# Kernel optimization log

Measured on AMD Instinct MI355X. Metric: run time of the kernel, lower is better.

The kernel has to match this reference:

```python
import jax, jax.numpy as jnp
import numpy as np

K = 6            # kmer length
NF = 8192        # n_filters (> 4**K so kmer_params has shape (NF, 4, K))
M = 4 ** K       # 4096 kmers
B = 1024         # batch


def setup_inputs() -> dict:
    key = jax.random.key(0)
    k1, k2 = jax.random.split(key)
    freq = jax.random.uniform(k1, (B, M), dtype=jnp.float32)          # kmer frequencies (B, 4^k)
    kmer_params = jax.random.normal(k2, (NF, 4, K), dtype=jnp.float32)
    temperature = jnp.ones((1,), dtype=jnp.float32)
    # base-4 digits of arange(4^k), most-significant first == itertools.product order
    pos = 4 ** jnp.arange(K - 1, -1, -1)
    kmer_idcs = ((jnp.arange(M)[:, None] // pos[None, :]) % 4).astype(jnp.int32)  # (M, K)
    return {"freq": freq, "kmer_params": kmer_params,
            "temperature": temperature, "kmer_idcs": kmer_idcs}


def reference(freq, kmer_params, temperature, kmer_idcs):
    k = kmer_params.shape[-1]
    # matches[f, i] = sum_j kmer_params[f, kmer_idcs[i, j], j]
    # Advanced indexing broadcasts (M, k) indices against arange(k): result (F, M, k).
    # This replaces torch's expand-to-(F, M, 1, k) + gather + squeeze + sum(-1).
    matches = kmer_params[:, kmer_idcs, jnp.arange(k)].sum(axis=-1)   # (F, M)
    probs = jax.nn.softmax(matches / temperature, axis=1)             # softmax over kmers
    pooled = freq @ probs.T                                           # (B, F)
    profile = pooled / pooled.sum(axis=1, keepdims=True)
    return profile
```

## Files before the change

### kernel.cpp

```cpp
#include <hip/hip_runtime.h>


typedef __bf16  bf16x8 __attribute__((ext_vector_type(8)));
typedef float   f32x4  __attribute__((ext_vector_type(4)));

#define GLD16(gp, lp)                                                          \
  __builtin_amdgcn_global_load_lds(                                            \
      (const __attribute__((address_space(1))) void*)(gp),                     \
      (__attribute__((address_space(3))) void*)(lp), 16, 0, 0)

__device__ __forceinline__ short f2bf(float x) {
  unsigned u = __float_as_uint(x);
  unsigned r = (u + 0x7fffu + ((u >> 16) & 1u)) >> 16;
  return (short)r;
}

__device__ __forceinline__ float wave_max(float v) {
  #pragma unroll
  for (int off = 32; off; off >>= 1) v = fmaxf(v, __shfl_xor(v, off, 64));
  return v;
}
__device__ __forceinline__ float wave_sum(float v) {
  #pragma unroll
  for (int off = 32; off; off >>= 1) v += __shfl_xor(v, off, 64);
  return v;
}

__global__ __launch_bounds__(256) void cast_kernel(const float* __restrict__ in,
                                                   short* __restrict__ out) {
  int idx = blockIdx.x * 256 + threadIdx.x;
  float4 v = ((const float4*)in)[idx];
  short4 o;
  o.x = f2bf(v.x); o.y = f2bf(v.y); o.z = f2bf(v.z); o.w = f2bf(v.w);
  ((short4*)out)[idx] = o;
}

__global__ __launch_bounds__(256) void tables_kernel(const float* __restrict__ kp,
                                                     const float* __restrict__ temp,
                                                     float* __restrict__ E1t,
                                                     float* __restrict__ E2) {
  const int t = threadIdx.x;
  const int lane = t & 63, wave = t >> 6;
  const int f = blockIdx.x * 4 + wave;
  const float* P = kp + f * 24;
  const int d0 = (lane >> 4) & 3, d1 = (lane >> 2) & 3, d2 = lane & 3;
  const float thi = P[d0 * 6 + 0] + P[d1 * 6 + 1] + P[d2 * 6 + 2];
  const float tlo = P[d0 * 6 + 3] + P[d1 * 6 + 4] + P[d2 * 6 + 5];
  const float mxhi = wave_max(thi), mxlo = wave_max(tlo);
  const float invT = 1.0f / temp[0];
  const float e1 = __expf((thi - mxhi) * invT);
  const float e2 = __expf((tlo - mxlo) * invT);
  const float s1 = wave_sum(e1), s2 = wave_sum(e2);
  const float invZ = 1.0f / (s1 * s2);
  E1t[lane * 8192 + f] = e1 * invZ;
  E2[(size_t)f * 64 + lane] = e2;
}

__global__ __launch_bounds__(256, 4) void gemm_kernel(const short* __restrict__ A,
                                                      const float* __restrict__ E1t,
                                                      const float* __restrict__ E2,
                                                      float* __restrict__ C) {
  __shared__ short As[64 * 64];

  const int t = threadIdx.x;
  const int lane = t & 63, wave = t >> 6;
  const int quad = lane >> 4, l16 = lane & 15;
  const int m0 = blockIdx.y * 64;
  const int n0 = blockIdx.x * 128;
  const int wn = wave * 32;

  f32x4 acc[4][2];
  #pragma unroll
  for (int i = 0; i < 4; i++)
    #pragma unroll
    for (int j = 0; j < 2; j++) acc[i][j] = (f32x4){0.f, 0.f, 0.f, 0.f};

  int nrow[2];
  #pragma unroll
  for (int j = 0; j < 2; j++) nrow[j] = n0 + wn + j * 16 + l16;
  float4 e2a[2][2], e2b[2][2];
  #pragma unroll
  for (int j = 0; j < 2; j++)
    #pragma unroll
    for (int ks = 0; ks < 2; ks++) {
      const float* p = E2 + (size_t)nrow[j] * 64 + (ks * 4 + quad) * 8;
      e2a[j][ks] = *(const float4*)p;
      e2b[j][ks] = *(const float4*)(p + 4);
    }

  const int lane_row = lane >> 3;
  const int src_col = ((lane & 7) ^ lane_row) * 8;
  const int sw = l16 & 7;

  for (int kt = 0; kt < 64; kt++) {
    const int kofs = kt * 64;
    float e1v[2];
    #pragma unroll
    for (int j = 0; j < 2; j++) e1v[j] = E1t[kt * 8192 + nrow[j]];

    __syncthreads();
    #pragma unroll
    for (int c = 0; c < 2; c++) {
      const int chunk = wave * 2 + c;
      const int row = chunk * 8 + lane_row;
      GLD16(A + (m0 + row) * 4096 + kofs + src_col, &As[chunk * 512 + lane * 8]);
    }
    __syncthreads();

    bf16x8 b[2][2];
    #pragma unroll
    for (int j = 0; j < 2; j++)
      #pragma unroll
      for (int ks = 0; ks < 2; ks++) {
        const float s = e1v[j];
        bf16x8 bb;
        bb[0] = (__bf16)(s * e2a[j][ks].x);
        bb[1] = (__bf16)(s * e2a[j][ks].y);
        bb[2] = (__bf16)(s * e2a[j][ks].z);
        bb[3] = (__bf16)(s * e2a[j][ks].w);
        bb[4] = (__bf16)(s * e2b[j][ks].x);
        bb[5] = (__bf16)(s * e2b[j][ks].y);
        bb[6] = (__bf16)(s * e2b[j][ks].z);
        bb[7] = (__bf16)(s * e2b[j][ks].w);
        b[ks][j] = bb;
      }

    #pragma unroll
    for (int ks = 0; ks < 2; ks++) {
      const int pcol = ((ks * 4 + quad) ^ sw) * 8;
      bf16x8 a[4];
      #pragma unroll
      for (int i = 0; i < 4; i++)
        a[i] = *(const bf16x8*)&As[(i * 16 + l16) * 64 + pcol];
      #pragma unroll
      for (int i = 0; i < 4; i++)
        #pragma unroll
        for (int j = 0; j < 2; j++)
          acc[i][j] = __builtin_amdgcn_mfma_f32_16x16x32_bf16(a[i], b[ks][j], acc[i][j], 0, 0, 0);
    }
  }

  #pragma unroll
  for (int i = 0; i < 4; i++) {
    #pragma unroll
    for (int r = 0; r < 4; r++) {
      const int brow = m0 + i * 16 + quad * 4 + r;
      float* crow = C + (size_t)brow * 8192 + n0 + wn + l16;
      #pragma unroll
      for (int j = 0; j < 2; j++) crow[j * 16] = acc[i][j][r];
    }
  }
}

__global__ __launch_bounds__(256) void norm_kernel(float* __restrict__ out) {
  const int b = blockIdx.x;
  const int t = threadIdx.x;
  const int lane = t & 63, wave = t >> 6;
  __shared__ float red[4];

  float4* row = (float4*)(out + (size_t)b * 8192);
  float4 v[8];
  float s = 0.0f;
  #pragma unroll
  for (int q = 0; q < 8; q++) {
    v[q] = row[q * 256 + t];
    s += (v[q].x + v[q].y) + (v[q].z + v[q].w);
  }
  float ws = wave_sum(s);
  if (lane == 0) red[wave] = ws;
  __syncthreads();
  float tot = (red[0] + red[1]) + (red[2] + red[3]);
  float inv = 1.0f / tot;
  #pragma unroll
  for (int q = 0; q < 8; q++) {
    v[q].x *= inv; v[q].y *= inv; v[q].z *= inv; v[q].w *= inv;
    row[q * 256 + t] = v[q];
  }
}

extern "C" void kernel_launch(void* const* d_in, const int* in_sizes, int n_in,
                              void* d_out, int out_size, void* d_ws, size_t ws_size,
                              hipStream_t stream) {
  const float* freq    = (const float*)d_in[0];
  const float* kparams = (const float*)d_in[1];
  const float* temp    = (const float*)d_in[2];

  float* out = (float*)d_out;

  short* freqb = (short*)d_ws;
  float* E1t   = (float*)(freqb + (size_t)1024 * 4096);
  float* E2    = E1t + (size_t)64 * 8192;

  cast_kernel  <<<4096, 256, 0, stream>>>(freq, freqb);
  tables_kernel<<<2048, 256, 0, stream>>>(kparams, temp, E1t, E2);
  gemm_kernel  <<<dim3(64, 16), 256, 0, stream>>>(freqb, E1t, E2, out);
  norm_kernel  <<<1024, 256, 0, stream>>>(out);
}
```

Baseline: 162.1 us.

## Precompute row denominators algebraically and fuse normalization into GEMM epilogue

Merges the cast and table kernels into one prep kernel that also computes per-block partial column sums of the bf16-rounded probability matrix. A new denom kernel reduces these sums and dots them with each freq row to get the row normalizer ahead of time. The GEMM then scales its output directly, so the separate norm pass that re-read and rewrote the 32MB output disappears. The cost is an extra small kernel with only 64 blocks and an extra reduction inside prep. The normalizer is now computed from rounded values rather than from the GEMM output, so it may differ slightly from the actual row sums.

```diff
diff --git a/kernel.cpp b/kernel.cpp
--- a/kernel.cpp
+++ b/kernel.cpp
@@ -14,6 +14,14 @@
   unsigned r = (u + 0x7fffu + ((u >> 16) & 1u)) >> 16;
   return (short)r;
 }
+__device__ __forceinline__ float bf_round(float x) {
+  unsigned u = __float_as_uint(x);
+  unsigned r = (u + 0x7fffu + ((u >> 16) & 1u)) & 0xffff0000u;
+  return __uint_as_float(r);
+}
+__device__ __forceinline__ float bf2f(unsigned short u) {
+  return __uint_as_float(((unsigned)u) << 16);
+}
 
 __device__ __forceinline__ float wave_max(float v) {
   #pragma unroll
@@ -26,39 +34,134 @@
   return v;
 }
 
-__global__ __launch_bounds__(256) void cast_kernel(const float* __restrict__ in,
-                                                   short* __restrict__ out) {
-  int idx = blockIdx.x * 256 + threadIdx.x;
-  float4 v = ((const float4*)in)[idx];
-  short4 o;
-  o.x = f2bf(v.x); o.y = f2bf(v.y); o.z = f2bf(v.z); o.w = f2bf(v.w);
-  ((short4*)out)[idx] = o;
-}
-
-__global__ __launch_bounds__(256) void tables_kernel(const float* __restrict__ kp,
-                                                     const float* __restrict__ temp,
-                                                     float* __restrict__ E1t,
-                                                     float* __restrict__ E2) {
+__global__ __launch_bounds__(256) void prep_kernel(const float* __restrict__ freq,
+                                                   const float* __restrict__ kp,
+                                                   const float* __restrict__ temp,
+                                                   short* __restrict__ freqb,
+                                                   float* __restrict__ E1t,
+                                                   float* __restrict__ E2,
+                                                   float* __restrict__ S_part) {
+  __shared__ float E1loc[64][64];
+  __shared__ float E2loc[64][64];
+  const int blk = blockIdx.x;
   const int t = threadIdx.x;
+
+  if (blk < 4096) {
+    int idx = blk * 256 + t;
+    float4 v = ((const float4*)freq)[idx];
+    short4 o;
+    o.x = f2bf(v.x); o.y = f2bf(v.y); o.z = f2bf(v.z); o.w = f2bf(v.w);
+    ((short4*)freqb)[idx] = o;
+    return;
+  }
+
+  const int bb = blk - 4096;
+  const int f0 = bb * 64;
   const int lane = t & 63, wave = t >> 6;
-  const int f = blockIdx.x * 4 + wave;
-  const float* P = kp + f * 24;
+  const float invT = 1.0f / temp[0];
   const int d0 = (lane >> 4) & 3, d1 = (lane >> 2) & 3, d2 = lane & 3;
-  const float thi = P[d0 * 6 + 0] + P[d1 * 6 + 1] + P[d2 * 6 + 2];
-  const float tlo = P[d0 * 6 + 3] + P[d1 * 6 + 4] + P[d2 * 6 + 5];
-  const float mxhi = wave_max(thi), mxlo = wave_max(tlo);
-  const float invT = 1.0f / temp[0];
-  const float e1 = __expf((thi - mxhi) * invT);
-  const float e2 = __expf((tlo - mxlo) * invT);
-  const float s1 = wave_sum(e1), s2 = wave_sum(e2);
-  const float invZ = 1.0f / (s1 * s2);
-  E1t[lane * 8192 + f] = e1 * invZ;
-  E2[(size_t)f * 64 + lane] = e2;
+
+  #pragma unroll
+  for (int ffi = 0; ffi < 16; ffi++) {
+    const int floc = wave * 16 + ffi;
+    const float* P = kp + (size_t)(f0 + floc) * 24;
+    const float thi = P[d0 * 6 + 0] + P[d1 * 6 + 1] + P[d2 * 6 + 2];
+    const float tlo = P[d0 * 6 + 3] + P[d1 * 6 + 4] + P[d2 * 6 + 5];
+    const float mxhi = wave_max(thi), mxlo = wave_max(tlo);
+    const float e1 = __expf((thi - mxhi) * invT);
+    const float e2 = __expf((tlo - mxlo) * invT);
+    const float s1 = wave_sum(e1), s2 = wave_sum(e2);
+    const float invZ = 1.0f / (s1 * s2);
+    E1loc[floc][lane] = e1 * invZ;
+    E2loc[floc][lane] = e2;
+  }
+  __syncthreads();
+
+  {
+    const int h = t >> 2, lb = (t & 3) * 16;
+    float acc[16];
+    #pragma unroll
+    for (int ll = 0; ll < 16; ll++) acc[ll] = 0.0f;
+    for (int ff = 0; ff < 64; ff++) {
+      const float a = E1loc[ff][h];
+      #pragma unroll
+      for (int ll = 0; ll < 16; ll++)
+        acc[ll] += bf_round(a * E2loc[ff][lb + ll]);
+    }
+    float* dst = S_part + (size_t)bb * 4096 + h * 64 + lb;
+    #pragma unroll
+    for (int q = 0; q < 4; q++)
+      ((f32x4*)dst)[q] = (f32x4){acc[q*4], acc[q*4+1], acc[q*4+2], acc[q*4+3]};
+  }
+
+  {
+    const int h = t >> 2, c0 = (t & 3) * 16;
+    float tmp[16];
+    #pragma unroll
+    for (int cc = 0; cc < 16; cc++) tmp[cc] = E1loc[c0 + cc][h];
+    float* dst = E1t + (size_t)h * 8192 + f0 + c0;
+    #pragma unroll
+    for (int q = 0; q < 4; q++)
+      ((f32x4*)dst)[q] = (f32x4){tmp[q*4], tmp[q*4+1], tmp[q*4+2], tmp[q*4+3]};
+  }
+
+  {
+    const int fl = t >> 2, l0 = (t & 3) * 16;
+    float* dst = E2 + (size_t)(f0 + fl) * 64 + l0;
+    #pragma unroll
+    for (int q = 0; q < 4; q++)
+      ((f32x4*)dst)[q] = *(const f32x4*)&E2loc[fl][l0 + q * 4];
+  }
+}
+
+__global__ __launch_bounds__(256) void denom_kernel(const short* __restrict__ freqb,
+                                                    const float* __restrict__ S_part,
+                                                    float* __restrict__ invDenom) {
+  __shared__ float Svec[4096];
+  const int t = threadIdx.x;
+  const int b0 = blockIdx.x * 16;
+
+  {
+    const int i0 = t * 16;
+    float acc[16];
+    #pragma unroll
+    for (int q = 0; q < 16; q++) acc[q] = 0.0f;
+    for (int p = 0; p < 128; p++) {
+      const f32x4* src = (const f32x4*)(S_part + (size_t)p * 4096 + i0);
+      #pragma unroll
+      for (int q = 0; q < 4; q++) {
+        f32x4 v = src[q];
+        acc[q*4+0] += v.x; acc[q*4+1] += v.y; acc[q*4+2] += v.z; acc[q*4+3] += v.w;
+      }
+    }
+    #pragma unroll
+    for (int q = 0; q < 4; q++)
+      ((f32x4*)(Svec + i0))[q] = (f32x4){acc[q*4], acc[q*4+1], acc[q*4+2], acc[q*4+3]};
+  }
+  __syncthreads();
+
+  const int lane = t & 63, wave = t >> 6;
+  #pragma unroll
+  for (int rr = 0; rr < 4; rr++) {
+    const int row = b0 + wave * 4 + rr;
+    const unsigned short* fr = (const unsigned short*)(freqb + (size_t)row * 4096);
+    float s = 0.0f;
+    #pragma unroll
+    for (int ch = 0; ch < 16; ch++) {
+      const int i = ch * 256 + lane * 4;
+      ushort4 u = *(const ushort4*)(fr + i);
+      f32x4 sv = *(const f32x4*)(Svec + i);
+      s += bf2f(u.x) * sv.x + bf2f(u.y) * sv.y + bf2f(u.z) * sv.z + bf2f(u.w) * sv.w;
+    }
+    const float tot = wave_sum(s);
+    if (lane == 0) invDenom[row] = 1.0f / tot;
+  }
 }
 
 __global__ __launch_bounds__(256, 4) void gemm_kernel(const short* __restrict__ A,
                                                       const float* __restrict__ E1t,
                                                       const float* __restrict__ E2,
+                                                      const float* __restrict__ invDenom,
                                                       float* __restrict__ C) {
   __shared__ short As[64 * 64];
 
@@ -140,6 +243,13 @@
     }
   }
 
+  float invd[4][4];
+  #pragma unroll
+  for (int i = 0; i < 4; i++)
+    #pragma unroll
+    for (int r = 0; r < 4; r++)
+      invd[i][r] = invDenom[m0 + i * 16 + quad * 4 + r];
+
   #pragma unroll
   for (int i = 0; i < 4; i++) {
     #pragma unroll
@@ -147,34 +257,8 @@
       const int brow = m0 + i * 16 + quad * 4 + r;
       float* crow = C + (size_t)brow * 8192 + n0 + wn + l16;
       #pragma unroll
-      for (int j = 0; j < 2; j++) crow[j * 16] = acc[i][j][r];
-    }
-  }
-}
-
-__global__ __launch_bounds__(256) void norm_kernel(float* __restrict__ out) {
-  const int b = blockIdx.x;
-  const int t = threadIdx.x;
-  const int lane = t & 63, wave = t >> 6;
-  __shared__ float red[4];
-
-  float4* row = (float4*)(out + (size_t)b * 8192);
-  float4 v[8];
-  float s = 0.0f;
-  #pragma unroll
-  for (int q = 0; q < 8; q++) {
-    v[q] = row[q * 256 + t];
-    s += (v[q].x + v[q].y) + (v[q].z + v[q].w);
-  }
-  float ws = wave_sum(s);
-  if (lane == 0) red[wave] = ws;
-  __syncthreads();
-  float tot = (red[0] + red[1]) + (red[2] + red[3]);
-  float inv = 1.0f / tot;
-  #pragma unroll
-  for (int q = 0; q < 8; q++) {
-    v[q].x *= inv; v[q].y *= inv; v[q].z *= inv; v[q].w *= inv;
-    row[q * 256 + t] = v[q];
+      for (int j = 0; j < 2; j++) crow[j * 16] = acc[i][j][r] * invd[i][r];
+    }
   }
 }
 
@@ -190,9 +274,10 @@
   short* freqb = (short*)d_ws;
   float* E1t   = (float*)(freqb + (size_t)1024 * 4096);
   float* E2    = E1t + (size_t)64 * 8192;
-
-  cast_kernel  <<<4096, 256, 0, stream>>>(freq, freqb);
-  tables_kernel<<<2048, 256, 0, stream>>>(kparams, temp, E1t, E2);
-  gemm_kernel  <<<dim3(64, 16), 256, 0, stream>>>(freqb, E1t, E2, out);
-  norm_kernel  <<<1024, 256, 0, stream>>>(out);
-}
+  float* S_part = E2 + (size_t)8192 * 64;
+  float* invDenom = S_part + (size_t)128 * 4096;
+
+  prep_kernel <<<4224, 256, 0, stream>>>(freq, kparams, temp, freqb, E1t, E2, S_part);
+  denom_kernel<<<64, 256, 0, stream>>>(freqb, S_part, invDenom);
+  gemm_kernel <<<dim3(64, 16), 256, 0, stream>>>(freqb, E1t, E2, invDenom, out);
+}
```

New measurement: 228.7 us. 41.1% more time.

## Fuse cast and table kernels, coalesce E1t writes, deepen GEMM K-tile

Applied to the files above, without the earlier changes.

Merges the bf16 cast and the softmax-table kernels into one launch. Table blocks now handle 64 filters each and stage the results in shared memory so the transposed E1t writes go out as coalesced vector stores. The GEMM K-tile grows from 64 to 256, which cuts the number of barrier pairs and per-iteration global loads by four. In exchange it uses four times the LDS (32KB) and lowers the launch-bounds occupancy hint to 3.

```diff
diff --git a/kernel.cpp b/kernel.cpp
--- a/kernel.cpp
+++ b/kernel.cpp
@@ -26,41 +26,73 @@
   return v;
 }
 
-__global__ __launch_bounds__(256) void cast_kernel(const float* __restrict__ in,
-                                                   short* __restrict__ out) {
-  int idx = blockIdx.x * 256 + threadIdx.x;
-  float4 v = ((const float4*)in)[idx];
-  short4 o;
-  o.x = f2bf(v.x); o.y = f2bf(v.y); o.z = f2bf(v.z); o.w = f2bf(v.w);
-  ((short4*)out)[idx] = o;
-}
-
-__global__ __launch_bounds__(256) void tables_kernel(const float* __restrict__ kp,
-                                                     const float* __restrict__ temp,
-                                                     float* __restrict__ E1t,
-                                                     float* __restrict__ E2) {
+__global__ __launch_bounds__(256) void prep_kernel(const float* __restrict__ freq,
+                                                   const float* __restrict__ kp,
+                                                   const float* __restrict__ temp,
+                                                   short* __restrict__ freqb,
+                                                   float* __restrict__ E1t,
+                                                   float* __restrict__ E2) {
+  __shared__ float E1loc[64][64];
+  __shared__ float E2loc[64][64];
+  const int blk = blockIdx.x;
   const int t = threadIdx.x;
+
+  if (blk < 4096) {
+    int idx = blk * 256 + t;
+    float4 v = ((const float4*)freq)[idx];
+    short4 o;
+    o.x = f2bf(v.x); o.y = f2bf(v.y); o.z = f2bf(v.z); o.w = f2bf(v.w);
+    ((short4*)freqb)[idx] = o;
+    return;
+  }
+
+  const int bb = blk - 4096;
+  const int f0 = bb * 64;
   const int lane = t & 63, wave = t >> 6;
-  const int f = blockIdx.x * 4 + wave;
-  const float* P = kp + f * 24;
+  const float invT = 1.0f / temp[0];
   const int d0 = (lane >> 4) & 3, d1 = (lane >> 2) & 3, d2 = lane & 3;
-  const float thi = P[d0 * 6 + 0] + P[d1 * 6 + 1] + P[d2 * 6 + 2];
-  const float tlo = P[d0 * 6 + 3] + P[d1 * 6 + 4] + P[d2 * 6 + 5];
-  const float mxhi = wave_max(thi), mxlo = wave_max(tlo);
-  const float invT = 1.0f / temp[0];
-  const float e1 = __expf((thi - mxhi) * invT);
-  const float e2 = __expf((tlo - mxlo) * invT);
-  const float s1 = wave_sum(e1), s2 = wave_sum(e2);
-  const float invZ = 1.0f / (s1 * s2);
-  E1t[lane * 8192 + f] = e1 * invZ;
-  E2[(size_t)f * 64 + lane] = e2;
-}
-
-__global__ __launch_bounds__(256, 4) void gemm_kernel(const short* __restrict__ A,
+
+  #pragma unroll
+  for (int ffi = 0; ffi < 16; ffi++) {
+    const int floc = wave * 16 + ffi;
+    const float* P = kp + (size_t)(f0 + floc) * 24;
+    const float thi = P[d0 * 6 + 0] + P[d1 * 6 + 1] + P[d2 * 6 + 2];
+    const float tlo = P[d0 * 6 + 3] + P[d1 * 6 + 4] + P[d2 * 6 + 5];
+    const float mxhi = wave_max(thi), mxlo = wave_max(tlo);
+    const float e1 = __expf((thi - mxhi) * invT);
+    const float e2 = __expf((tlo - mxlo) * invT);
+    const float s1 = wave_sum(e1), s2 = wave_sum(e2);
+    const float invZ = 1.0f / (s1 * s2);
+    E1loc[floc][lane] = e1 * invZ;
+    E2loc[floc][lane] = e2;
+  }
+  __syncthreads();
+
+  {
+    const int h = t >> 2, c0 = (t & 3) * 16;
+    float tmp[16];
+    #pragma unroll
+    for (int cc = 0; cc < 16; cc++) tmp[cc] = E1loc[c0 + cc][h];
+    float* dst = E1t + (size_t)h * 8192 + f0 + c0;
+    #pragma unroll
+    for (int q = 0; q < 4; q++)
+      ((f32x4*)dst)[q] = (f32x4){tmp[q*4], tmp[q*4+1], tmp[q*4+2], tmp[q*4+3]};
+  }
+
+  {
+    const int fl = t >> 2, l0 = (t & 3) * 16;
+    float* dst = E2 + (size_t)(f0 + fl) * 64 + l0;
+    #pragma unroll
+    for (int q = 0; q < 4; q++)
+      ((f32x4*)dst)[q] = *(const f32x4*)&E2loc[fl][l0 + q * 4];
+  }
+}
+
+__global__ __launch_bounds__(256, 3) void gemm_kernel(const short* __restrict__ A,
                                                       const float* __restrict__ E1t,
                                                       const float* __restrict__ E2,
                                                       float* __restrict__ C) {
-  __shared__ short As[64 * 64];
+  __shared__ short As[64 * 256];
 
   const int t = threadIdx.x;
   const int lane = t & 63, wave = t >> 6;
@@ -78,65 +110,72 @@
   int nrow[2];
   #pragma unroll
   for (int j = 0; j < 2; j++) nrow[j] = n0 + wn + j * 16 + l16;
+
   float4 e2a[2][2], e2b[2][2];
   #pragma unroll
   for (int j = 0; j < 2; j++)
     #pragma unroll
-    for (int ks = 0; ks < 2; ks++) {
-      const float* p = E2 + (size_t)nrow[j] * 64 + (ks * 4 + quad) * 8;
-      e2a[j][ks] = *(const float4*)p;
-      e2b[j][ks] = *(const float4*)(p + 4);
-    }
-
-  const int lane_row = lane >> 3;
-  const int src_col = ((lane & 7) ^ lane_row) * 8;
+    for (int par = 0; par < 2; par++) {
+      const float* p = E2 + (size_t)nrow[j] * 64 + par * 32 + quad * 8;
+      e2a[j][par] = *(const float4*)p;
+      e2b[j][par] = *(const float4*)(p + 4);
+    }
+
+  const int lrow_half = lane >> 5;
+  const int pblk = lane & 31;
   const int sw = l16 & 7;
 
-  for (int kt = 0; kt < 64; kt++) {
-    const int kofs = kt * 64;
-    float e1v[2];
-    #pragma unroll
-    for (int j = 0; j < 2; j++) e1v[j] = E1t[kt * 8192 + nrow[j]];
+  for (int kt = 0; kt < 16; kt++) {
+    const int kofs = kt * 256;
+
+    float e1v[2][4];
+    #pragma unroll
+    for (int hh = 0; hh < 4; hh++)
+      #pragma unroll
+      for (int j = 0; j < 2; j++)
+        e1v[j][hh] = E1t[(kt * 4 + hh) * 8192 + nrow[j]];
 
     __syncthreads();
     #pragma unroll
-    for (int c = 0; c < 2; c++) {
-      const int chunk = wave * 2 + c;
-      const int row = chunk * 8 + lane_row;
+    for (int c = 0; c < 8; c++) {
+      const int chunk = wave * 8 + c;
+      const int row = chunk * 2 + lrow_half;
+      const int src_col = (pblk ^ (row & 7)) * 8;
       GLD16(A + (m0 + row) * 4096 + kofs + src_col, &As[chunk * 512 + lane * 8]);
     }
     __syncthreads();
 
-    bf16x8 b[2][2];
-    #pragma unroll
-    for (int j = 0; j < 2; j++)
-      #pragma unroll
-      for (int ks = 0; ks < 2; ks++) {
-        const float s = e1v[j];
+    #pragma unroll
+    for (int ks = 0; ks < 8; ks++) {
+      const int q = ks * 4 + quad;
+      const int pcol = (q ^ sw) * 8;
+      bf16x8 a[4];
+      #pragma unroll
+      for (int i = 0; i < 4; i++)
+        a[i] = *(const bf16x8*)&As[(i * 16 + l16) * 256 + pcol];
+
+      const int hh = ks >> 1, par = ks & 1;
+      bf16x8 b[2];
+      #pragma unroll
+      for (int j = 0; j < 2; j++) {
+        const float s = e1v[j][hh];
         bf16x8 bb;
-        bb[0] = (__bf16)(s * e2a[j][ks].x);
-        bb[1] = (__bf16)(s * e2a[j][ks].y);
-        bb[2] = (__bf16)(s * e2a[j][ks].z);
-        bb[3] = (__bf16)(s * e2a[j][ks].w);
-        bb[4] = (__bf16)(s * e2b[j][ks].x);
-        bb[5] = (__bf16)(s * e2b[j][ks].y);
-        bb[6] = (__bf16)(s * e2b[j][ks].z);
-        bb[7] = (__bf16)(s * e2b[j][ks].w);
-        b[ks][j] = bb;
+        bb[0] = (__bf16)(s * e2a[j][par].x);
+        bb[1] = (__bf16)(s * e2a[j][par].y);
+        bb[2] = (__bf16)(s * e2a[j][par].z);
+        bb[3] = (__bf16)(s * e2a[j][par].w);
+        bb[4] = (__bf16)(s * e2b[j][par].x);
+        bb[5] = (__bf16)(s * e2b[j][par].y);
+        bb[6] = (__bf16)(s * e2b[j][par].z);
+        bb[7] = (__bf16)(s * e2b[j][par].w);
+        b[j] = bb;
       }
 
-    #pragma unroll
-    for (int ks = 0; ks < 2; ks++) {
-      const int pcol = ((ks * 4 + quad) ^ sw) * 8;
-      bf16x8 a[4];
-      #pragma unroll
-      for (int i = 0; i < 4; i++)
-        a[i] = *(const bf16x8*)&As[(i * 16 + l16) * 64 + pcol];
       #pragma unroll
       for (int i = 0; i < 4; i++)
         #pragma unroll
         for (int j = 0; j < 2; j++)
-          acc[i][j] = __builtin_amdgcn_mfma_f32_16x16x32_bf16(a[i], b[ks][j], acc[i][j], 0, 0, 0);
+          acc[i][j] = __builtin_amdgcn_mfma_f32_16x16x32_bf16(a[i], b[j], acc[i][j], 0, 0, 0);
     }
   }
 
@@ -191,8 +230,7 @@
   float* E1t   = (float*)(freqb + (size_t)1024 * 4096);
   float* E2    = E1t + (size_t)64 * 8192;
 
-  cast_kernel  <<<4096, 256, 0, stream>>>(freq, freqb);
-  tables_kernel<<<2048, 256, 0, stream>>>(kparams, temp, E1t, E2);
-  gemm_kernel  <<<dim3(64, 16), 256, 0, stream>>>(freqb, E1t, E2, out);
-  norm_kernel  <<<1024, 256, 0, stream>>>(out);
-}
+  prep_kernel<<<4224, 256, 0, stream>>>(freq, kparams, temp, freqb, E1t, E2);
+  gemm_kernel<<<dim3(64, 16), 256, 0, stream>>>(freqb, E1t, E2, out);
+  norm_kernel<<<1024, 256, 0, stream>>>(out);
+}
```

New measurement: 181.2 us. +11.8%, slower.
